# Kernel tuning notes

Measured on AMD Instinct MI355X. Metric: run time of the kernel, lower is better.

Reference implementation:

```python
import jax, jax.numpy as jnp
import numpy as np
from jax import lax

HID = 896          # hidden_size
HALF = HID // 2    # 448
BINS = 256         # 2 ** (bits/2), bits=16
B, T = 16, 2048


def setup_inputs() -> dict:
    key = jax.random.key(0)
    ks = jax.random.split(key, 16)
    rn = lambda k, shape, s: (jax.random.normal(k, shape, jnp.float32) * s)
    inp = {
        'conditional': jax.random.normal(ks[0], (B, T, 3, HID), jnp.float32),
        'input_signal': jax.random.randint(ks[1], (B, T, 2), 0, BINS, jnp.int32),
        'target_coarse': jax.random.randint(ks[2], (B, T, 1), 0, BINS, jnp.int32),
        # project_coarse_input: Linear(2, 3*half, bias=False)
        'Wc': rn(ks[3], (2, 3 * HALF), 0.5),
        # project_fine_input: Linear(3, 3*half, bias=False)
        'Wf': rn(ks[4], (3, 3 * HALF), 0.5),
        # stripped GRU hidden-to-hidden weights/biases (input projection is rnn_input itself)
        'W_hh': rn(ks[5], (HID, 3 * HID), 0.02),
        'b_ih': jnp.zeros((3 * HID,), jnp.float32),
        'b_hh': jnp.zeros((3 * HID,), jnp.float32),
        # to_bins_coarse: Linear(half, half) + ReLU + Linear(half, bins)
        'W1c': rn(ks[6], (HALF, HALF), 0.05), 'b1c': jnp.zeros((HALF,), jnp.float32),
        'W2c': rn(ks[7], (HALF, BINS), 0.05), 'b2c': jnp.zeros((BINS,), jnp.float32),
        # to_bins_fine
        'W1f': rn(ks[8], (HALF, HALF), 0.05), 'b1f': jnp.zeros((HALF,), jnp.float32),
        'W2f': rn(ks[9], (HALF, BINS), 0.05), 'b2f': jnp.zeros((BINS,), jnp.float32),
    }
    return inp


def _scale(x):
    # [0, BINS-1] -> [-1, 1]
    return x.astype(jnp.float32) / ((BINS - 1) / 2.0) - 1.0


def reference(conditional, input_signal, target_coarse, Wc, Wf, W_hh, b_ih, b_hh,
              W1c, b1c, W2c, b2c, W1f, b1f, W2f, b2f):
    sig = _scale(input_signal)          # [B, T, 2]
    tc = _scale(target_coarse)          # [B, T, 1]

    coarse_proj = (sig @ Wc).reshape(B, T, 3, HALF)
    fine_proj = (jnp.concatenate([sig, tc], axis=2) @ Wf).reshape(B, T, 3, HALF)
    # concat along feature halves -> [B, T, 3, HID], add conditional, flatten gates
    rnn_input = jnp.concatenate([coarse_proj, fine_proj], axis=3) + conditional
    rnn_input = rnn_input.reshape(B, T, 3 * HID) + b_ih
    xs = rnn_input.transpose(1, 0, 2)   # [T, B, 3*HID]

    def step(h, x_t):
        gh = h @ W_hh + b_hh                      # [B, 3*HID]
        xr, xz, xn = jnp.split(x_t, 3, axis=-1)
        hr, hz, hn = jnp.split(gh, 3, axis=-1)
        r = jax.nn.sigmoid(xr + hr)
        z = jax.nn.sigmoid(xz + hz)
        n = jnp.tanh(xn + r * hn)
        h_new = (1.0 - z) * n + z * h
        return h_new, h_new

    h0 = jnp.zeros((B, HID), jnp.float32)
    last_hidden, hidden_states = lax.scan(step, h0, xs)   # [T, B, HID]
    hidden_states = hidden_states.transpose(1, 0, 2)      # [B, T, HID]

    hidden_coarse = hidden_states[..., :HALF]
    # NOTE: original code applies to_bins_fine to hidden_coarse as well (faithful).
    out_coarse = jax.nn.relu(hidden_coarse @ W1c + b1c) @ W2c + b2c
    out_fine = jax.nn.relu(hidden_coarse @ W1f + b1f) @ W2f + b2f
    return out_coarse, out_fine, last_hidden
```

## Files before the change

### kernel.cpp

```cpp
#include <hip/hip_runtime.h>
#include <hip/hip_cooperative_groups.h>

namespace cg = cooperative_groups;

#define BB 16
#define TT 2048
#define HIDN 896
#define HALFN 448
#define NBINS 256
#define NWG 112
#define NTHR 64
#define WSTR 904

typedef __attribute__((ext_vector_type(8))) short short8;
typedef __attribute__((ext_vector_type(4))) float f32x4;
typedef __attribute__((ext_vector_type(2))) unsigned long long ull2;

__device__ __forceinline__ unsigned short f2bf(float x) {
    unsigned int u = __float_as_uint(x);
    unsigned int r = u + 0x7FFFu + ((u >> 16) & 1u);
    return (unsigned short)(r >> 16);
}

__global__ __launch_bounds__(NTHR, 1)
void scan_kernel(const float* __restrict__ cond,
                 const int*   __restrict__ sig,
                 const int*   __restrict__ tcrs,
                 const float* __restrict__ Wc,
                 const float* __restrict__ Wf,
                 const float* __restrict__ Whh,
                 const float* __restrict__ b_ih,
                 const float* __restrict__ b_hh,
                 unsigned long long* __restrict__ hx,
                 int* __restrict__ slots,
                 unsigned short* __restrict__ hc_out,
                 float* __restrict__ lasth)
{
    __shared__ unsigned short sW[32 * WSTR];

    const int tid  = threadIdx.x;
    const int wg   = blockIdx.x;
    const int col0 = wg * 8;

    for (int idx = tid; idx < 32 * HIDN; idx += NTHR) {
        int j2 = idx & 31, k = idx >> 5;
        unsigned short wv = 0;
        if (j2 < 16)
            wv = f2bf(Whh[(size_t)k * 2688 + (j2 >> 3) * HIDN + col0 + (j2 & 7)]);
        else if (j2 < 24)
            wv = f2bf(Whh[(size_t)k * 2688 + 2 * HIDN + col0 + (j2 & 7)]);
        sW[j2 * WSTR + k] = wv;
    }
    if (tid == 0)
        __hip_atomic_store(&slots[wg * 16], 0, __ATOMIC_RELAXED, __HIP_MEMORY_SCOPE_AGENT);

    const int l  = tid;
    const int q  = l & 15;
    const int hi = l >> 4;
    const int gA   = q >> 3;
    const int colA = col0 + (q & 7);

    float wpA0, wpA1, wpA2, wpB0, wpB1, wpB2;
    if (colA < HALFN) {
        wpA0 = Wc[gA * HALFN + colA];
        wpA1 = Wc[1344 + gA * HALFN + colA];
        wpA2 = 0.f;
        wpB0 = Wc[2 * HALFN + colA];
        wpB1 = Wc[1344 + 2 * HALFN + colA];
        wpB2 = 0.f;
    } else {
        int ck = colA - HALFN;
        wpA0 = Wf[gA * HALFN + ck];
        wpA1 = Wf[1344 + gA * HALFN + ck];
        wpA2 = Wf[2688 + gA * HALFN + ck];
        wpB0 = Wf[2 * HALFN + ck];
        wpB1 = Wf[1344 + 2 * HALFN + ck];
        wpB2 = Wf[2688 + 2 * HALFN + ck];
    }
    const float biA = b_ih[gA * HIDN + colA];
    const float bhA = b_hh[gA * HIDN + colA];
    const float biB = b_ih[2 * HIDN + colA];
    const float bhB = b_hh[2 * HIDN + colA];

    float hp[4] = {0.f, 0.f, 0.f, 0.f};

    __syncthreads();
    cg::this_grid().sync();

    const float inv = 1.f / 127.5f;
    const int zsrc = (l & 48) | 8 | (q & 7);

#define WAITS(s) { bool ok_;                                                   \
    for (;;) {                                                                 \
        ok_ = true;                                                            \
        if (l < 28) {                                                          \
            int a_ = __hip_atomic_load(&slots[((s)*28 + l) * 16],              \
                __ATOMIC_RELAXED, __HIP_MEMORY_SCOPE_AGENT);                   \
            ok_ = (a_ >= t);                                                   \
        }                                                                      \
        if (__all(ok_)) break;                                                 \
        __builtin_amdgcn_s_sleep(1);                                           \
    }                                                                          \
    asm volatile("" ::: "memory"); }

#define LOADF(s, V) _Pragma("unroll")                                          \
    for (int i_ = 0; i_ < 7; ++i_) {                                           \
        _Pragma("unroll")                                                      \
        for (int h_ = 0; h_ < 2; ++h_)                                         \
            V[2*i_ + h_] = __hip_atomic_load(                                  \
                &hb[(size_t)(4 * ((s)*7 + i_) + hi) * 32 + h_ * 16 + q],       \
                __ATOMIC_RELAXED, __HIP_MEMORY_SCOPE_AGENT);                   \
    }

#define MFMAS(s, V) _Pragma("unroll")                                          \
    for (int i_ = 0; i_ < 7; ++i_) {                                           \
        ull2 tv_; tv_.x = V[2*i_]; tv_.y = V[2*i_ + 1];                        \
        short8 av_ = __builtin_bit_cast(short8, tv_);                          \
        int ks_ = (s)*7 + i_;                                                  \
        short8 b1_ = *(const short8*)&sW[q * WSTR + hi * 8 + ks_ * 32];        \
        chA[ks_ & 3] = __builtin_amdgcn_mfma_f32_16x16x32_bf16(                \
            av_, b1_, chA[ks_ & 3], 0, 0, 0);                                  \
        short8 b2_ = *(const short8*)&sW[(16 + q) * WSTR + hi * 8 + ks_ * 32]; \
        chB[ks_ & 3] = __builtin_amdgcn_mfma_f32_16x16x32_bf16(                \
            av_, b2_, chB[ks_ & 3], 0, 0, 0);                                  \
    }

    for (int t = 0; t < TT; ++t) {
        float xcA[4], xcB[4], sg0[4], sg1[4], sg2[4];
        #pragma unroll
        for (int r = 0; r < 4; ++r) {
            int b = hi * 4 + r;
            size_t bt = (size_t)b * TT + t;
            xcA[r] = cond[(bt * 3 + gA) * HIDN + colA];
            xcB[r] = cond[(bt * 3 + 2) * HIDN + colA];
            sg0[r] = (float)sig[bt * 2 + 0] * inv - 1.f;
            sg1[r] = (float)sig[bt * 2 + 1] * inv - 1.f;
            sg2[r] = (float)tcrs[bt] * inv - 1.f;
        }

        f32x4 chA[4] = {}, chB[4] = {};
        if (t > 0) {
            const unsigned long long* hb = hx + (size_t)(t & 1) * 3584;
            unsigned long long va[14], vb[14];
            WAITS(0); LOADF(0, va);
            WAITS(1); LOADF(1, vb);
            MFMAS(0, va);
            WAITS(2); LOADF(2, va);
            MFMAS(1, vb);
            WAITS(3); LOADF(3, vb);
            MFMAS(2, va);
            MFMAS(3, vb);
        }
        f32x4 aA = (chA[0] + chA[1]) + (chA[2] + chA[3]);
        f32x4 aB = (chB[0] + chB[1]) + (chB[2] + chB[3]);

        float xvA[4], xvB[4], sigA[4];
        #pragma unroll
        for (int r = 0; r < 4; ++r) {
            xvA[r] = xcA[r] + biA + sg0[r]*wpA0 + sg1[r]*wpA1 + sg2[r]*wpA2;
            xvB[r] = xcB[r] + biB + sg0[r]*wpB0 + sg1[r]*wpB1 + sg2[r]*wpB2;
            sigA[r] = 1.f / (1.f + __expf(-(xvA[r] + aA[r] + bhA)));
        }
        float hnv[4];
        unsigned short hbits[4] = {0, 0, 0, 0};
        #pragma unroll
        for (int r = 0; r < 4; ++r) {
            float zz = __shfl(sigA[r], zsrc);
            float a2v = xvB[r] + sigA[r] * (aB[r] + bhB);
            float e = __expf(-2.f * a2v);
            float n = (1.f - e) / (1.f + e);
            float hn = (1.f - zz) * n + zz * hp[r];
            hnv[r] = hn;
            if (q < 8) { hp[r] = hn; hbits[r] = f2bf(hn); }
        }
        if (t == TT - 1 && q < 8) {
            #pragma unroll
            for (int r = 0; r < 4; ++r)
                lasth[(size_t)(hi * 4 + r) * HIDN + colA] = hnv[r];
        }

        unsigned p32[4];
        unsigned long long hv64[4];
        #pragma unroll
        for (int r = 0; r < 4; ++r) {
            int o1 = __shfl_xor((int)(unsigned)hbits[r], 1);
            p32[r] = ((unsigned)hbits[r] & 0xffffu) | ((unsigned)o1 << 16);
            int o2 = __shfl_xor((int)p32[r], 2);
            hv64[r] = (unsigned long long)p32[r] |
                      ((unsigned long long)(unsigned)o2 << 32);
        }
        if (t < TT - 1 && (q == 0 || q == 4)) {
            unsigned long long* hd = hx + (size_t)((t + 1) & 1) * 3584;
            #pragma unroll
            for (int r = 0; r < 4; ++r)
                __hip_atomic_store(&hd[(size_t)wg * 32 + (q >> 2) * 16 + hi * 4 + r],
                                   hv64[r], __ATOMIC_RELAXED, __HIP_MEMORY_SCOPE_AGENT);
        }
        asm volatile("s_waitcnt vmcnt(0)" ::: "memory");
        if (tid == 0)
            __hip_atomic_store(&slots[wg * 16], t + 1,
                               __ATOMIC_RELAXED, __HIP_MEMORY_SCOPE_AGENT);

        if (wg < 56 && q < 8 && !(q & 1)) {
            unsigned* hc32 = (unsigned*)hc_out;
            #pragma unroll
            for (int r = 0; r < 4; ++r)
                hc32[((size_t)(hi * 4 + r) * TT + t) * 224 + wg * 4 + (q >> 1)] = p32[r];
        }
    }
#undef WAITS
#undef LOADF
#undef MFMAS
}

template<int RELU_BF16>
__global__ __launch_bounds__(256)
void head_gemm(const unsigned short* __restrict__ A,
               const float* __restrict__ Bw,
               const float* __restrict__ bias,
               unsigned short* __restrict__ Cb,
               float* __restrict__ Cf,
               int N)
{
    const int K = 448;
    __shared__ float As[32][68];
    __shared__ float Bs[32][68];
    const int tid = threadIdx.x;
    const int tx = tid & 15;
    const int ty = tid >> 4;
    const int bm = blockIdx.x * 64;
    const int bn = blockIdx.y * 64;

    float acc[4][4] = {};

    for (int k0 = 0; k0 < K; k0 += 32) {
        #pragma unroll
        for (int it = 0; it < 2; ++it) {
            int idx = tid + it * 256;
            int m   = idx >> 3;
            int k4  = idx & 7;
            ushort4 av = *(const ushort4*)(A + (size_t)(bm + m) * K + k0 + k4 * 4);
            As[k4 * 4 + 0][m] = __uint_as_float((unsigned)av.x << 16);
            As[k4 * 4 + 1][m] = __uint_as_float((unsigned)av.y << 16);
            As[k4 * 4 + 2][m] = __uint_as_float((unsigned)av.z << 16);
            As[k4 * 4 + 3][m] = __uint_as_float((unsigned)av.w << 16);
        }
        #pragma unroll
        for (int it = 0; it < 2; ++it) {
            int idx = tid + it * 256;
            int k   = idx >> 4;
            int n4  = idx & 15;
            *(float4*)&Bs[k][n4 * 4] =
                *(const float4*)(Bw + (size_t)(k0 + k) * N + bn + n4 * 4);
        }
        __syncthreads();
        #pragma unroll
        for (int k = 0; k < 32; ++k) {
            float4 a4 = *(float4*)&As[k][ty * 4];
            float4 b4 = *(float4*)&Bs[k][tx * 4];
            float ar[4] = {a4.x, a4.y, a4.z, a4.w};
            float br[4] = {b4.x, b4.y, b4.z, b4.w};
            #pragma unroll
            for (int i = 0; i < 4; ++i)
                #pragma unroll
                for (int j = 0; j < 4; ++j)
                    acc[i][j] = fmaf(ar[i], br[j], acc[i][j]);
        }
        __syncthreads();
    }

    float4 bsv = *(const float4*)(bias + bn + tx * 4);
    float bb[4] = {bsv.x, bsv.y, bsv.z, bsv.w};
    #pragma unroll
    for (int i = 0; i < 4; ++i) {
        int row = bm + ty * 4 + i;
        float v[4];
        #pragma unroll
        for (int j = 0; j < 4; ++j) v[j] = acc[i][j] + bb[j];
        if (RELU_BF16) {
            ushort4 o;
            o.x = f2bf(fmaxf(v[0], 0.f));
            o.y = f2bf(fmaxf(v[1], 0.f));
            o.z = f2bf(fmaxf(v[2], 0.f));
            o.w = f2bf(fmaxf(v[3], 0.f));
            *(ushort4*)(Cb + (size_t)row * N + bn + tx * 4) = o;
        } else {
            float4 o = make_float4(v[0], v[1], v[2], v[3]);
            *(float4*)(Cf + (size_t)row * N + bn + tx * 4) = o;
        }
    }
}

extern "C" void kernel_launch(void* const* d_in, const int* in_sizes, int n_in,
                              void* d_out, int out_size, void* d_ws, size_t ws_size,
                              hipStream_t stream)
{
    const float* cond = (const float*)d_in[0];
    const int*   sig  = (const int*)d_in[1];
    const int*   tcrs = (const int*)d_in[2];
    const float* Wc   = (const float*)d_in[3];
    const float* Wf   = (const float*)d_in[4];
    const float* Whh  = (const float*)d_in[5];
    const float* bih  = (const float*)d_in[6];
    const float* bhh  = (const float*)d_in[7];
    const float* W1c  = (const float*)d_in[8];
    const float* b1c  = (const float*)d_in[9];
    const float* W2c  = (const float*)d_in[10];
    const float* b2c  = (const float*)d_in[11];
    const float* W1f  = (const float*)d_in[12];
    const float* b1f  = (const float*)d_in[13];
    const float* W2f  = (const float*)d_in[14];
    const float* b2f  = (const float*)d_in[15];

    char* ws = (char*)d_ws;
    int* slots               = (int*)ws;
    unsigned long long* hx   = (unsigned long long*)(ws + 8192);
    unsigned short* hc       = (unsigned short*)(ws + 65536);
    unsigned short* hid1     = (unsigned short*)(ws + 65536 + 29360128);

    float* outc  = (float*)d_out;
    float* outf  = outc + (size_t)BB * TT * NBINS;
    float* lasth = outc + 2 * (size_t)BB * TT * NBINS;

    void* args[] = {(void*)&cond, (void*)&sig, (void*)&tcrs, (void*)&Wc, (void*)&Wf,
                    (void*)&Whh, (void*)&bih, (void*)&bhh,
                    (void*)&hx, (void*)&slots, (void*)&hc, (void*)&lasth};
    hipLaunchCooperativeKernel((void*)scan_kernel, dim3(NWG), dim3(NTHR),
                               args, 0, stream);

    dim3 blk(256);
    head_gemm<1><<<dim3(512, 7), blk, 0, stream>>>(hc,   W1c, b1c, hid1, nullptr, 448);
    head_gemm<0><<<dim3(512, 4), blk, 0, stream>>>(hid1, W2c, b2c, nullptr, outc, 256);
    head_gemm<1><<<dim3(512, 7), blk, 0, stream>>>(hc,   W1f, b1f, hid1, nullptr, 448);
    head_gemm<0><<<dim3(512, 4), blk, 0, stream>>>(hid1, W2f, b2f, nullptr, outf, 256);
}
```

Measured before the change: 9.249 ms.

## Replace staged per-chunk waits with single all-slot wait and remap column blocks

Each workgroup now waits once for all 112 producer slots before loading the full hidden state, instead of waiting on four groups of 28 slots interleaved with the loads and MFMAs. Workgroups are also remapped to column blocks with a strided permutation (wg&7)*14 + (wg>>3), likely to spread neighbouring columns across XCDs. The single wait cuts the number of polling loops, but it gives up overlap between the early chunk MFMAs and the later chunks' arrivals.

```diff
diff --git a/kernel.cpp b/kernel.cpp
--- a/kernel.cpp
+++ b/kernel.cpp
@@ -40,7 +40,8 @@
 
     const int tid  = threadIdx.x;
     const int wg   = blockIdx.x;
-    const int col0 = wg * 8;
+    const int cb   = (wg & 7) * 14 + (wg >> 3);
+    const int col0 = cb * 8;
 
     for (int idx = tid; idx < 32 * HIDN; idx += NTHR) {
         int j2 = idx & 31, k = idx >> 5;
@@ -90,20 +91,19 @@
     const float inv = 1.f / 127.5f;
     const int zsrc = (l & 48) | 8 | (q & 7);
 
-#define WAITS(s) { bool ok_;                                                   \
+#define WAITALL(t) { bool ok_;                                                 \
     for (;;) {                                                                 \
-        ok_ = true;                                                            \
-        if (l < 28) {                                                          \
-            int a_ = __hip_atomic_load(&slots[((s)*28 + l) * 16],              \
-                __ATOMIC_RELAXED, __HIP_MEMORY_SCOPE_AGENT);                   \
-            ok_ = (a_ >= t);                                                   \
-        }                                                                      \
+        int a_ = __hip_atomic_load(&slots[l * 16],                             \
+            __ATOMIC_RELAXED, __HIP_MEMORY_SCOPE_AGENT);                       \
+        int b_ = (l < 48) ? __hip_atomic_load(&slots[(l + 64) * 16],           \
+            __ATOMIC_RELAXED, __HIP_MEMORY_SCOPE_AGENT) : a_;                  \
+        ok_ = (a_ >= (t)) & (b_ >= (t));                                       \
         if (__all(ok_)) break;                                                 \
         __builtin_amdgcn_s_sleep(1);                                           \
     }                                                                          \
     asm volatile("" ::: "memory"); }
 
-#define LOADF(s, V) _Pragma("unroll")                                          \
+#define LOADH(s, V) _Pragma("unroll")                                          \
     for (int i_ = 0; i_ < 7; ++i_) {                                           \
         _Pragma("unroll")                                                      \
         for (int h_ = 0; h_ < 2; ++h_)                                         \
@@ -140,14 +140,15 @@
 
         f32x4 chA[4] = {}, chB[4] = {};
         if (t > 0) {
+            WAITALL(t);
             const unsigned long long* hb = hx + (size_t)(t & 1) * 3584;
             unsigned long long va[14], vb[14];
-            WAITS(0); LOADF(0, va);
-            WAITS(1); LOADF(1, vb);
+            LOADH(0, va);
+            LOADH(1, vb);
             MFMAS(0, va);
-            WAITS(2); LOADF(2, va);
+            LOADH(2, va);
             MFMAS(1, vb);
-            WAITS(3); LOADF(3, vb);
+            LOADH(3, vb);
             MFMAS(2, va);
             MFMAS(3, vb);
         }
@@ -193,7 +194,7 @@
             unsigned long long* hd = hx + (size_t)((t + 1) & 1) * 3584;
             #pragma unroll
             for (int r = 0; r < 4; ++r)
-                __hip_atomic_store(&hd[(size_t)wg * 32 + (q >> 2) * 16 + hi * 4 + r],
+                __hip_atomic_store(&hd[(size_t)cb * 32 + (q >> 2) * 16 + hi * 4 + r],
                                    hv64[r], __ATOMIC_RELAXED, __HIP_MEMORY_SCOPE_AGENT);
         }
         asm volatile("s_waitcnt vmcnt(0)" ::: "memory");
@@ -201,15 +202,15 @@
             __hip_atomic_store(&slots[wg * 16], t + 1,
                                __ATOMIC_RELAXED, __HIP_MEMORY_SCOPE_AGENT);
 
-        if (wg < 56 && q < 8 && !(q & 1)) {
+        if (cb < 56 && q < 8 && !(q & 1)) {
             unsigned* hc32 = (unsigned*)hc_out;
             #pragma unroll
             for (int r = 0; r < 4; ++r)
-                hc32[((size_t)(hi * 4 + r) * TT + t) * 224 + wg * 4 + (q >> 1)] = p32[r];
-        }
-    }
-#undef WAITS
-#undef LOADF
+                hc32[((size_t)(hi * 4 + r) * TT + t) * 224 + cb * 4 + (q >> 1)] = p32[r];
+        }
+    }
+#undef WAITALL
+#undef LOADH
 #undef MFMAS
 }
 
```

New measurement: 8.178 ms. 1.13x faster.
